# Performance work log

Measured on AMD Instinct MI355X. Metric: run time of the kernel, lower is better.

Reference implementation:

```python
import jax, jax.numpy as jnp
import numpy as np
from jax import lax

FH, FW = 5, 5  # filter_width, filter_height


def setup_inputs() -> dict:
    key = jax.random.key(0)
    k_in, k_f, k_b = jax.random.split(key, 3)
    return {
        "input": jax.random.normal(k_in, (8192, 8192), dtype=jnp.float32),
        "filter": jax.random.normal(k_f, (FH, FW), dtype=jnp.float32),
        "bias": jax.random.normal(k_b, (1, 1), dtype=jnp.float32),
    }


def reference(input, filter, bias):
    # Splat conv: out[i+di, j+dj] += input[i,j] * filter[di,dj]
    # == TRUE convolution with FULL padding -> output (H+FH-1, W+FW-1).
    # lax.conv does cross-correlation, so flip the filter in both spatial dims.
    fh, fw = filter.shape
    x = input[None, None]                      # NCHW, [1,1,H,W]
    k = jnp.flip(filter, (0, 1))[None, None]   # OIHW, [1,1,fh,fw]
    out = lax.conv_general_dilated(
        x, k,
        window_strides=(1, 1),
        padding=[(fh - 1, fh - 1), (fw - 1, fw - 1)],
        dimension_numbers=("NCHW", "OIHW", "NCHW"),
    )
    # Note: the original forward does NOT add bias (bias is only saved for bwd).
    return out[0, 0]
```

## Files before the change

kernel.cpp:

```cpp
#include <hip/hip_runtime.h>


#define IN_H 8192
#define IN_W 8192
#define OUT_H 8196
#define OUT_W 8196
#define NG 2049

__global__ __launch_bounds__(256) void splat_conv_kernel(
    const float* __restrict__ in, const float* __restrict__ flt,
    float* __restrict__ out) {
  const int g = blockIdx.x * 64 + threadIdx.x;
  const int row = blockIdx.y * 4 + threadIdx.y;
  if (g >= NG) return;

  float f[25];
#pragma unroll
  for (int i = 0; i < 25; ++i) f[i] = flt[i];

  const int c0 = 4 * g - 4;
  const bool lo_ok = (g != 0);
  const bool hi_ok = (g != NG - 1);

  float acc0 = 0.f, acc1 = 0.f, acc2 = 0.f, acc3 = 0.f;

#pragma unroll
  for (int dr = 0; dr < 5; ++dr) {
    const int r = row + dr - 4;
    float4 a = make_float4(0.f, 0.f, 0.f, 0.f);
    float4 b = make_float4(0.f, 0.f, 0.f, 0.f);
    if (r >= 0 && r < IN_H) {
      const float* rp = in + (size_t)r * IN_W;
      if (lo_ok) a = *(const float4*)(rp + c0);
      if (hi_ok) b = *(const float4*)(rp + c0 + 4);
    }
    float x[8];
    x[0] = a.x; x[1] = a.y; x[2] = a.z; x[3] = a.w;
    x[4] = b.x; x[5] = b.y; x[6] = b.z; x[7] = b.w;

    const int di = 4 - dr;
#pragma unroll
    for (int dj = 0; dj < 5; ++dj) {
      const float w = f[di * 5 + dj];
      acc0 += x[0 + 4 - dj] * w;
      acc1 += x[1 + 4 - dj] * w;
      acc2 += x[2 + 4 - dj] * w;
      acc3 += x[3 + 4 - dj] * w;
    }
  }

  float4 o = make_float4(acc0, acc1, acc2, acc3);
  *(float4*)(out + (size_t)row * OUT_W + 4 * g) = o;
}

extern "C" void kernel_launch(void* const* d_in, const int* in_sizes, int n_in,
                              void* d_out, int out_size, void* d_ws,
                              size_t ws_size, hipStream_t stream) {
  const float* in = (const float*)d_in[0];
  const float* flt = (const float*)d_in[1];
  float* out = (float*)d_out;

  dim3 block(64, 4);
  dim3 grid((NG + 63) / 64, OUT_H / 4);
  splat_conv_kernel<<<grid, block, 0, stream>>>(in, flt, out);
}
```

Baseline: 506.4 us.

## Compute 4x4 output tile per thread with interior fast path

Each thread now produces four output rows instead of one, loading eight input rows once and reusing them in registers across the four rows. A separate branch-free path handles interior tiles, while edge tiles keep the bounds checks. This cuts redundant global loads and index math per output, at the cost of more registers and fewer threads in flight.

```diff
diff --git a/kernel.cpp b/kernel.cpp
--- a/kernel.cpp
+++ b/kernel.cpp
@@ -6,51 +6,88 @@
 #define OUT_H 8196
 #define OUT_W 8196
 #define NG 2049
+#define NRG 2049
 
 __global__ __launch_bounds__(256) void splat_conv_kernel(
     const float* __restrict__ in, const float* __restrict__ flt,
     float* __restrict__ out) {
   const int g = blockIdx.x * 64 + threadIdx.x;
-  const int row = blockIdx.y * 4 + threadIdx.y;
-  if (g >= NG) return;
+  const int rg = blockIdx.y * 4 + threadIdx.y;
+  if (g >= NG || rg >= NRG) return;
 
   float f[25];
 #pragma unroll
   for (int i = 0; i < 25; ++i) f[i] = flt[i];
 
+  const int orow = rg * 4;
   const int c0 = 4 * g - 4;
-  const bool lo_ok = (g != 0);
-  const bool hi_ok = (g != NG - 1);
 
-  float acc0 = 0.f, acc1 = 0.f, acc2 = 0.f, acc3 = 0.f;
+  float acc[4][4];
+#pragma unroll
+  for (int k = 0; k < 4; ++k)
+#pragma unroll
+    for (int m = 0; m < 4; ++m) acc[k][m] = 0.f;
 
+  const bool interior = (g >= 1) & (g <= NG - 2) & (rg >= 1) & (rg <= 2047);
+
+  if (interior) {
+    const float* rp = in + (size_t)(orow - 4) * IN_W + c0;
 #pragma unroll
-  for (int dr = 0; dr < 5; ++dr) {
-    const int r = row + dr - 4;
-    float4 a = make_float4(0.f, 0.f, 0.f, 0.f);
-    float4 b = make_float4(0.f, 0.f, 0.f, 0.f);
-    if (r >= 0 && r < IN_H) {
-      const float* rp = in + (size_t)r * IN_W;
-      if (lo_ok) a = *(const float4*)(rp + c0);
-      if (hi_ok) b = *(const float4*)(rp + c0 + 4);
+    for (int rr = 0; rr < 8; ++rr) {
+      const float4 a = *(const float4*)(rp);
+      const float4 b = *(const float4*)(rp + 4);
+      rp += IN_W;
+      float x[8];
+      x[0] = a.x; x[1] = a.y; x[2] = a.z; x[3] = a.w;
+      x[4] = b.x; x[5] = b.y; x[6] = b.z; x[7] = b.w;
+#pragma unroll
+      for (int k = 0; k < 4; ++k) {
+        const int di = k + 4 - rr;
+        if (di < 0 || di > 4) continue;
+#pragma unroll
+        for (int dj = 0; dj < 5; ++dj) {
+          const float w = f[di * 5 + dj];
+#pragma unroll
+          for (int m = 0; m < 4; ++m) acc[k][m] += x[m + 4 - dj] * w;
+        }
+      }
     }
-    float x[8];
-    x[0] = a.x; x[1] = a.y; x[2] = a.z; x[3] = a.w;
-    x[4] = b.x; x[5] = b.y; x[6] = b.z; x[7] = b.w;
-
-    const int di = 4 - dr;
+  } else {
+    const bool lo_ok = (g != 0);
+    const bool hi_ok = (g != NG - 1);
 #pragma unroll
-    for (int dj = 0; dj < 5; ++dj) {
-      const float w = f[di * 5 + dj];
-      acc0 += x[0 + 4 - dj] * w;
-      acc1 += x[1 + 4 - dj] * w;
-      acc2 += x[2 + 4 - dj] * w;
-      acc3 += x[3 + 4 - dj] * w;
+    for (int rr = 0; rr < 8; ++rr) {
+      const int r = orow - 4 + rr;
+      float4 a = make_float4(0.f, 0.f, 0.f, 0.f);
+      float4 b = make_float4(0.f, 0.f, 0.f, 0.f);
+      if (r >= 0 && r < IN_H) {
+        const float* rp = in + (size_t)r * IN_W + c0;
+        if (lo_ok) a = *(const float4*)(rp);
+        if (hi_ok) b = *(const float4*)(rp + 4);
+      }
+      float x[8];
+      x[0] = a.x; x[1] = a.y; x[2] = a.z; x[3] = a.w;
+      x[4] = b.x; x[5] = b.y; x[6] = b.z; x[7] = b.w;
+#pragma unroll
+      for (int k = 0; k < 4; ++k) {
+        const int di = k + 4 - rr;
+        if (di < 0 || di > 4) continue;
+#pragma unroll
+        for (int dj = 0; dj < 5; ++dj) {
+          const float w = f[di * 5 + dj];
+#pragma unroll
+          for (int m = 0; m < 4; ++m) acc[k][m] += x[m + 4 - dj] * w;
+        }
+      }
     }
   }
 
-  float4 o = make_float4(acc0, acc1, acc2, acc3);
-  *(float4*)(out + (size_t)row * OUT_W + 4 * g) = o;
+  float* op = out + (size_t)orow * OUT_W + 4 * g;
+#pragma unroll
+  for (int k = 0; k < 4; ++k) {
+    *(float4*)(op) = make_float4(acc[k][0], acc[k][1], acc[k][2], acc[k][3]);
+    op += OUT_W;
+  }
 }
 
 extern "C" void kernel_launch(void* const* d_in, const int* in_sizes, int n_in,
@@ -61,6 +98,6 @@
   float* out = (float*)d_out;
 
   dim3 block(64, 4);
-  dim3 grid((NG + 63) / 64, OUT_H / 4);
+  dim3 grid((NG + 63) / 64, (NRG + 3) / 4);
   splat_conv_kernel<<<grid, block, 0, stream>>>(in, flt, out);
 }
```

Result: faster. 470.6 us (-7.1%).

## Stage input tile in LDS and compute four output rows per thread

Applied to the files above, without the earlier changes.

Each block now loads a 20x66 float4 input tile into shared memory once and each thread computes a 4x4 output patch (four rows) from it. This replaces the redundant per-thread global loads of the five input rows and cuts global traffic per output. Filter weights are also forced into scalar registers via readfirstlane. The change adds a barrier and LDS usage per block, and makes the grid 4x smaller in y, which could lower occupancy.

```diff
diff --git a/kernel.cpp b/kernel.cpp
--- a/kernel.cpp
+++ b/kernel.cpp
@@ -3,54 +3,90 @@
 
 #define IN_H 8192
 #define IN_W 8192
+#define IN_WG 2048
 #define OUT_H 8196
 #define OUT_W 8196
 #define NG 2049
+#define TROWS 16
+#define LDS_R 20
+#define LDS_C 66
+
+__device__ __forceinline__ float sgpr_f32(float v) {
+  return __int_as_float(__builtin_amdgcn_readfirstlane(__float_as_int(v)));
+}
 
 __global__ __launch_bounds__(256) void splat_conv_kernel(
     const float* __restrict__ in, const float* __restrict__ flt,
     float* __restrict__ out) {
-  const int g = blockIdx.x * 64 + threadIdx.x;
-  const int row = blockIdx.y * 4 + threadIdx.y;
-  if (g >= NG) return;
+  __shared__ float4 tile[LDS_R][LDS_C];
+
+  const int tx = threadIdx.x;
+  const int ty = threadIdx.y;
+  const int G0 = blockIdx.x * 64;
+  const int orow0 = blockIdx.y * TROWS;
 
   float f[25];
 #pragma unroll
-  for (int i = 0; i < 25; ++i) f[i] = flt[i];
+  for (int i = 0; i < 25; ++i) f[i] = sgpr_f32(flt[i]);
 
-  const int c0 = 4 * g - 4;
-  const bool lo_ok = (g != 0);
-  const bool hi_ok = (g != NG - 1);
+  {
+    const int igb = G0 - 1;
+#pragma unroll
+    for (int r = ty; r < LDS_R; r += 4) {
+      const int ir = orow0 - 4 + r;
+      const bool rok = (ir >= 0) & (ir < IN_H);
+      {
+        const int ig = igb + tx;
+        float4 v = make_float4(0.f, 0.f, 0.f, 0.f);
+        if (rok & (ig >= 0) & (ig < IN_WG))
+          v = *(const float4*)(in + (size_t)ir * IN_W + 4 * ig);
+        tile[r][tx] = v;
+      }
+      if (tx == 0) {
+        const int ig = igb + 64;
+        float4 v = make_float4(0.f, 0.f, 0.f, 0.f);
+        if (rok & (ig < IN_WG))
+          v = *(const float4*)(in + (size_t)ir * IN_W + 4 * ig);
+        tile[r][64] = v;
+      }
+    }
+  }
+  __syncthreads();
 
-  float acc0 = 0.f, acc1 = 0.f, acc2 = 0.f, acc3 = 0.f;
-
+  float acc[4][4] = {{0.f, 0.f, 0.f, 0.f}};
+  const int rbase = 4 * ty;
 #pragma unroll
-  for (int dr = 0; dr < 5; ++dr) {
-    const int r = row + dr - 4;
-    float4 a = make_float4(0.f, 0.f, 0.f, 0.f);
-    float4 b = make_float4(0.f, 0.f, 0.f, 0.f);
-    if (r >= 0 && r < IN_H) {
-      const float* rp = in + (size_t)r * IN_W;
-      if (lo_ok) a = *(const float4*)(rp + c0);
-      if (hi_ok) b = *(const float4*)(rp + c0 + 4);
-    }
+  for (int rr = 0; rr < 8; ++rr) {
+    const float4 a = tile[rbase + rr][tx];
+    const float4 b = tile[rbase + rr][tx + 1];
     float x[8];
     x[0] = a.x; x[1] = a.y; x[2] = a.z; x[3] = a.w;
     x[4] = b.x; x[5] = b.y; x[6] = b.z; x[7] = b.w;
-
-    const int di = 4 - dr;
 #pragma unroll
-    for (int dj = 0; dj < 5; ++dj) {
-      const float w = f[di * 5 + dj];
-      acc0 += x[0 + 4 - dj] * w;
-      acc1 += x[1 + 4 - dj] * w;
-      acc2 += x[2 + 4 - dj] * w;
-      acc3 += x[3 + 4 - dj] * w;
+    for (int k = 0; k < 4; ++k) {
+      const int di = k + 4 - rr;
+      if (di >= 0 && di <= 4) {
+#pragma unroll
+        for (int dj = 0; dj < 5; ++dj) {
+          const float w = f[di * 5 + dj];
+#pragma unroll
+          for (int m = 0; m < 4; ++m) acc[k][m] += x[m + 4 - dj] * w;
+        }
+      }
     }
   }
 
-  float4 o = make_float4(acc0, acc1, acc2, acc3);
-  *(float4*)(out + (size_t)row * OUT_W + 4 * g) = o;
+  const int g = G0 + tx;
+  if (g < NG) {
+    float* op = out + (size_t)(orow0 + 4 * ty) * OUT_W + 4 * g;
+#pragma unroll
+    for (int k = 0; k < 4; ++k) {
+      const int orow = orow0 + 4 * ty + k;
+      if (orow < OUT_H)
+        *(float4*)(op) = make_float4(acc[k][0], acc[k][1], acc[k][2], acc[k][3]);
+      op += OUT_W;
+    }
+  }
 }
 
 extern "C" void kernel_launch(void* const* d_in, const int* in_sizes, int n_in,
@@ -61,6 +97,6 @@
   float* out = (float*)d_out;
 
   dim3 block(64, 4);
-  dim3 grid((NG + 63) / 64, OUT_H / 4);
+  dim3 grid((NG + 63) / 64, (OUT_H + TROWS - 1) / TROWS);
   splat_conv_kernel<<<grid, block, 0, stream>>>(in, flt, out);
 }
```

New measurement: 472.5 us. -6.7%, faster.
